# Optimization experiments

Measured on AMD Instinct MI355X. Metric: run time of the kernel, lower is better.

The kernel has to match this reference:

```python
import jax, jax.numpy as jnp
import numpy as np

N_FEATURES = 1_000_000
N_FIELDS = 50
EMB_DIM = 64
ATT_DIM = EMB_DIM // 2
BATCH = 2048


def setup_inputs() -> dict:
    key = jax.random.key(0)
    ks = jax.random.split(key, 7)
    features = jax.random.randint(ks[0], (BATCH, N_FIELDS), 0, N_FEATURES)
    emb_table = jax.random.normal(ks[1], (N_FEATURES, EMB_DIM), dtype=jnp.float32) * 0.01
    coeff_table = jax.random.normal(ks[2], (N_FEATURES, 1), dtype=jnp.float32) * 0.01
    bias = jnp.zeros((1,), dtype=jnp.float32)
    # kaiming normal for relu: std = sqrt(2/fan_in)
    att_w = jax.random.normal(ks[3], (ATT_DIM, EMB_DIM), dtype=jnp.float32) * np.sqrt(2.0 / EMB_DIM)
    att_b = jnp.zeros((ATT_DIM,), dtype=jnp.float32)
    p = jax.random.normal(ks[4], (ATT_DIM, 1), dtype=jnp.float32)
    w = jnp.ones((EMB_DIM, 1), dtype=jnp.float32)
    return {"features": features, "emb_table": emb_table, "coeff_table": coeff_table,
            "bias": bias, "att_w": att_w, "att_b": att_b, "p": p, "w": w}


def reference(features, emb_table, coeff_table, bias, att_w, att_b, p, w):
    # Dropout layers in eval mode (identity).
    emb = emb_table[features]            # [B, F, D]
    coeff = coeff_table[features]        # [B, F, 1]
    iu, ju = jnp.triu_indices(N_FIELDS, k=1)
    # pairwise hadamard products in row-major (i,j) order matching the loop
    interactions = emb[:, iu, :] * emb[:, ju, :]   # [B, P, D], P = F*(F-1)/2
    # attention MLP: relu(x @ att_w^T + att_b) @ p -> scores over interactions
    hidden = jax.nn.relu(jnp.einsum('bpd,ad->bpa', interactions, att_w) + att_b)
    scores = jnp.einsum('bpa,ao->bpo', hidden, p)  # [B, P, 1]
    att = jax.nn.softmax(scores, axis=1)           # softmax over interaction dim
    pooled = jnp.sum(interactions * att, axis=1)   # [B, D]
    interaction_part = (pooled @ w).reshape(-1)    # [B]
    linear_part = jnp.sum(coeff, axis=1).reshape(-1)
    return interaction_part + linear_part + bias
```

## Files before the change

### kernel.cpp

```cpp
#include <hip/hip_runtime.h>
#include <hip/hip_fp16.h>
#include <math.h>

#define NFIELDS 50
#define EMBD 64
#define NPAIRS 1225
#define NTILEPAD 40
#define NPAD (NTILEPAD * 32)
#define NTHREADS 256
#define NWAVES 4
#define NITER (NTILEPAD / NWAVES)
#define QPT (NPAD / NTHREADS)
#define NFPAD 51

typedef _Float16 f16x8 __attribute__((ext_vector_type(8)));
typedef _Float16 f16x2 __attribute__((ext_vector_type(2)));
typedef float f32x16 __attribute__((ext_vector_type(16)));

union F16x8U { f16x8 v; f16x2 h2[4]; unsigned int u[4]; uint4 q; };
union U32F { unsigned int u; f16x2 h; };

__device__ __forceinline__ float dot2acc(f16x2 a, f16x2 b, float c) {
#if __has_builtin(__builtin_amdgcn_fdot2)
    return __builtin_amdgcn_fdot2(a, b, c, false);
#else
    return c + (float)a[0] * (float)b[0] + (float)a[1] * (float)b[1];
#endif
}

#define MNEG (-1e30f)

__launch_bounds__(NTHREADS, 4)
__global__ void afm_kernel(const int* __restrict__ features,
                           const float* __restrict__ emb_table,
                           const float* __restrict__ coeff_table,
                           const float* __restrict__ bias,
                           const float* __restrict__ att_w,
                           const float* __restrict__ att_b,
                           const float* __restrict__ pvec,
                           const float* __restrict__ wvec,
                           float* __restrict__ out)
{
    __shared__ __align__(16) unsigned short emb3[8][NFPAD][8];
    __shared__ unsigned short pair_s[NPAD];
    __shared__ int   feat_s[NFIELDS];
    __shared__ float red_m[NWAVES], red_s[NWAVES], red_st[NWAVES];
    __shared__ float red_csum;

    const int b    = blockIdx.x;
    const int tid  = threadIdx.x;
    const int lane = tid & 63;
    const int wid  = tid >> 6;
    const int col  = lane & 31;
    const int h    = lane >> 5;
    const int h4   = h * 4;

    int myfeat = 0;
    if (tid < NFIELDS) {
        myfeat = features[b * NFIELDS + tid];
        feat_s[tid] = myfeat;
    }

    #pragma unroll
    for (int k = 0; k < QPT; ++k) {
        const int q = tid * QPT + k;
        int i = 0, j = 1;
        if (q < NPAIRS) {
            const float s = sqrtf((float)(9801 - 8 * q));
            i = (int)((99.0f - s) * 0.5f);
            const int off = i * NFIELDS - ((i * (i + 1)) >> 1);
            j = i + 1 + (q - off);
        }
        pair_s[q] = (unsigned short)((i << 8) | j);
    }

    if (wid == 0) {
        float cacc = 0.f;
        if (tid < NFIELDS)       cacc = coeff_table[myfeat];
        else if (tid == NFIELDS) cacc = bias[0];
        #pragma unroll
        for (int m = 1; m < 64; m <<= 1) cacc += __shfl_xor(cacc, m, 64);
        if (tid == 0) red_csum = cacc;
    }

    f16x8 afragW[4];
    f16x2 w2[16];
    #pragma unroll
    for (int c = 0; c < 4; ++c) {
        const int d0 = c * 16 + h * 8;
        const float4 wa0 = *reinterpret_cast<const float4*>(&att_w[col * EMBD + d0]);
        const float4 wa1 = *reinterpret_cast<const float4*>(&att_w[col * EMBD + d0 + 4]);
        F16x8U bf;
        bf.v[0] = (_Float16)wa0.x; bf.v[1] = (_Float16)wa0.y;
        bf.v[2] = (_Float16)wa0.z; bf.v[3] = (_Float16)wa0.w;
        bf.v[4] = (_Float16)wa1.x; bf.v[5] = (_Float16)wa1.y;
        bf.v[6] = (_Float16)wa1.z; bf.v[7] = (_Float16)wa1.w;
        afragW[c] = bf.v;
        const float4 wv0 = *reinterpret_cast<const float4*>(&wvec[d0]);
        const float4 wv1 = *reinterpret_cast<const float4*>(&wvec[d0 + 4]);
        f16x2 t0; t0[0] = (_Float16)wv0.x; t0[1] = (_Float16)wv0.y; w2[c * 4 + 0] = t0;
        f16x2 t1; t1[0] = (_Float16)wv0.z; t1[1] = (_Float16)wv0.w; w2[c * 4 + 1] = t1;
        f16x2 t2; t2[0] = (_Float16)wv1.x; t2[1] = (_Float16)wv1.y; w2[c * 4 + 2] = t2;
        f16x2 t3; t3[0] = (_Float16)wv1.z; t3[1] = (_Float16)wv1.w; w2[c * 4 + 3] = t3;
    }
    float attb_r[16], p_r[16];
    #pragma unroll
    for (int reg = 0; reg < 16; ++reg) {
        const int r = (reg & 3) + 8 * (reg >> 2) + 4 * h;
        attb_r[reg] = att_b[r];
        p_r[reg]    = pvec[r];
    }
    __syncthreads();

    for (int idx = tid; idx < NFIELDS * 16; idx += NTHREADS) {
        const int f  = idx >> 4;
        const int d0 = (idx & 15) * 4;
        const float4 v = *reinterpret_cast<const float4*>(
            &emb_table[(size_t)feat_s[f] * EMBD + d0]);
        const int c  = d0 >> 4;
        const int hh = (d0 >> 3) & 1;
        const int e0 = d0 & 7;
        U32F t0, t1;
        t0.h[0] = (_Float16)v.x; t0.h[1] = (_Float16)v.y;
        t1.h[0] = (_Float16)v.z; t1.h[1] = (_Float16)v.w;
        uint2 pk; pk.x = t0.u; pk.y = t1.u;
        *reinterpret_cast<uint2*>(&emb3[hh * 4 + c][f][e0]) = pk;
    }
    __syncthreads();

    float m_run = MNEG, s_run = 0.f, st_run = 0.f;

    #pragma unroll 2
    for (int tt = 0; tt < NITER; ++tt) {
        const int tile = wid + tt * NWAVES;
        const int pidx = tile * 32 + col;
        const unsigned int ij = pair_s[pidx];
        const int fi = ij >> 8;
        const int fj = ij & 255;

        f32x16 acc;
        #pragma unroll
        for (int reg = 0; reg < 16; ++reg) acc[reg] = attb_r[reg];

        float t_half = 0.f;
        #pragma unroll
        for (int c = 0; c < 4; ++c) {
            F16x8U ai, aj;
            ai.q = *reinterpret_cast<const uint4*>(&emb3[h4 + c][fi][0]);
            aj.q = *reinterpret_cast<const uint4*>(&emb3[h4 + c][fj][0]);
            const f16x2 x0 = ai.h2[0] * aj.h2[0];
            const f16x2 x1 = ai.h2[1] * aj.h2[1];
            const f16x2 x2 = ai.h2[2] * aj.h2[2];
            const f16x2 x3 = ai.h2[3] * aj.h2[3];
            t_half = dot2acc(x0, w2[c * 4 + 0], t_half);
            t_half = dot2acc(x1, w2[c * 4 + 1], t_half);
            t_half = dot2acc(x2, w2[c * 4 + 2], t_half);
            t_half = dot2acc(x3, w2[c * 4 + 3], t_half);
            F16x8U bf;
            bf.h2[0] = x0; bf.h2[1] = x1; bf.h2[2] = x2; bf.h2[3] = x3;
            acc = __builtin_amdgcn_mfma_f32_32x32x16_f16(afragW[c], bf.v, acc, 0, 0, 0);
        }

        float sp = 0.f;
        #pragma unroll
        for (int reg = 0; reg < 16; ++reg)
            sp = fmaf(fmaxf(acc[reg], 0.f), p_r[reg], sp);
        const float sc = sp + __shfl_xor(sp, 32, 64);
        const float tf = t_half + __shfl_xor(t_half, 32, 64);

        const bool valid = (pidx < NPAIRS);
        const float scm = valid ? sc : MNEG;
        const float mn  = fmaxf(m_run, scm);
        const float scale = __expf(m_run - mn);
        const float e     = valid ? __expf(sc - mn) : 0.f;
        s_run  = s_run  * scale + e;
        st_run = st_run * scale + e * tf;
        m_run  = mn;
    }

    #pragma unroll
    for (int m = 1; m < 64; m <<= 1) {
        const float m2  = __shfl_xor(m_run, m, 64);
        const float s2  = __shfl_xor(s_run, m, 64);
        const float st2 = __shfl_xor(st_run, m, 64);
        const float mn  = fmaxf(m_run, m2);
        const float ea  = __expf(m_run - mn);
        const float eb  = __expf(m2 - mn);
        s_run  = s_run * ea + s2 * eb;
        st_run = st_run * ea + st2 * eb;
        m_run  = mn;
    }
    if (lane == 0) { red_m[wid] = m_run; red_s[wid] = s_run; red_st[wid] = st_run; }
    __syncthreads();

    if (tid == 0) {
        float M = red_m[0], S = red_s[0], ST = red_st[0];
        #pragma unroll
        for (int wq = 1; wq < NWAVES; ++wq) {
            const float mn = fmaxf(M, red_m[wq]);
            const float ea = __expf(M - mn);
            const float eb = __expf(red_m[wq] - mn);
            S  = S * ea + red_s[wq] * eb;
            ST = ST * ea + red_st[wq] * eb;
            M  = mn;
        }
        out[b] = ST / S + red_csum;
    }
}

extern "C" void kernel_launch(void* const* d_in, const int* in_sizes, int n_in,
                              void* d_out, int out_size, void* d_ws, size_t ws_size,
                              hipStream_t stream) {
    const int*   features    = (const int*)d_in[0];
    const float* emb_table   = (const float*)d_in[1];
    const float* coeff_table = (const float*)d_in[2];
    const float* bias        = (const float*)d_in[3];
    const float* att_w       = (const float*)d_in[4];
    const float* att_b       = (const float*)d_in[5];
    const float* pvec        = (const float*)d_in[6];
    const float* wvec        = (const float*)d_in[7];
    float* out = (float*)d_out;

    const int batch = in_sizes[0] / NFIELDS;
    afm_kernel<<<batch, NTHREADS, 0, stream>>>(
        features, emb_table, coeff_table, bias, att_w, att_b, pvec, wvec, out);
}
```

Before: 35.94 us.

## Prefetch next tile's LDS operands and pack score epilogue into fp16 dot2

Software-pipelines the main loop: the pair index and the embedding fragments for the next tile are loaded from LDS while the current tile's MFMA runs. This hides LDS latency, at the cost of more registers and unroll 1. The epilogue is also cut down. The ReLU·p reduction now uses packed fp16 dot2 after pkrtz conversion, and the score and weighted-sum halves are packed into one 32-bit value so a single cross-half shuffle replaces two. Rounding the partial sums to fp16 lowers precision in the softmax inputs.

```diff
diff --git a/kernel.cpp b/kernel.cpp
--- a/kernel.cpp
+++ b/kernel.cpp
@@ -12,13 +12,20 @@
 #define NITER (NTILEPAD / NWAVES)
 #define QPT (NPAD / NTHREADS)
 #define NFPAD 51
+#define CHSTR (NFPAD * 8)
 
 typedef _Float16 f16x8 __attribute__((ext_vector_type(8)));
 typedef _Float16 f16x2 __attribute__((ext_vector_type(2)));
+typedef __fp16   fp16x2 __attribute__((ext_vector_type(2)));
 typedef float f32x16 __attribute__((ext_vector_type(16)));
 
 union F16x8U { f16x8 v; f16x2 h2[4]; unsigned int u[4]; uint4 q; };
-union U32F { unsigned int u; f16x2 h; };
+union U32F { unsigned int u; f16x2 h; fp16x2 g; };
+
+__device__ __forceinline__ f16x2 pkrtz(float a, float b) {
+    U32F t; t.g = __builtin_amdgcn_cvt_pkrtz(a, b);
+    return t.h;
+}
 
 __device__ __forceinline__ float dot2acc(f16x2 a, f16x2 b, float c) {
 #if __has_builtin(__builtin_amdgcn_fdot2)
@@ -103,12 +110,19 @@
         f16x2 t2; t2[0] = (_Float16)wv1.x; t2[1] = (_Float16)wv1.y; w2[c * 4 + 2] = t2;
         f16x2 t3; t3[0] = (_Float16)wv1.z; t3[1] = (_Float16)wv1.w; w2[c * 4 + 3] = t3;
     }
-    float attb_r[16], p_r[16];
+    float attb_r[16];
+    f16x2 p16[8];
     #pragma unroll
     for (int reg = 0; reg < 16; ++reg) {
         const int r = (reg & 3) + 8 * (reg >> 2) + 4 * h;
         attb_r[reg] = att_b[r];
-        p_r[reg]    = pvec[r];
+    }
+    #pragma unroll
+    for (int q = 0; q < 8; ++q) {
+        const int r0 = ((2 * q) & 3) + 8 * ((2 * q) >> 2) + 4 * h;
+        const int r1 = ((2 * q + 1) & 3) + 8 * ((2 * q + 1) >> 2) + 4 * h;
+        f16x2 pp; pp[0] = (_Float16)pvec[r0]; pp[1] = (_Float16)pvec[r1];
+        p16[q] = pp;
     }
     __syncthreads();
 
@@ -128,15 +142,38 @@
     }
     __syncthreads();
 
+    const unsigned short* const ebase = &emb3[0][0][0] + h4 * CHSTR;
+
     float m_run = MNEG, s_run = 0.f, st_run = 0.f;
 
-    #pragma unroll 2
+    uint4 ai_c[4], aj_c[4];
+    int pidx_cur = wid * 32 + col;
+    {
+        const unsigned int ij = pair_s[pidx_cur];
+        const unsigned short* pi = ebase + (ij >> 8) * 8;
+        const unsigned short* pj = ebase + (ij & 255) * 8;
+        #pragma unroll
+        for (int c = 0; c < 4; ++c) {
+            ai_c[c] = *reinterpret_cast<const uint4*>(pi + c * CHSTR);
+            aj_c[c] = *reinterpret_cast<const uint4*>(pj + c * CHSTR);
+        }
+    }
+
+    #pragma unroll 1
     for (int tt = 0; tt < NITER; ++tt) {
-        const int tile = wid + tt * NWAVES;
-        const int pidx = tile * 32 + col;
-        const unsigned int ij = pair_s[pidx];
-        const int fi = ij >> 8;
-        const int fj = ij & 255;
+        const int ttn   = (tt + 1 < NITER) ? (tt + 1) : 0;
+        const int pidx_n = (wid + ttn * NWAVES) * 32 + col;
+        uint4 ai_n[4], aj_n[4];
+        {
+            const unsigned int ijn = pair_s[pidx_n];
+            const unsigned short* pin = ebase + (ijn >> 8) * 8;
+            const unsigned short* pjn = ebase + (ijn & 255) * 8;
+            #pragma unroll
+            for (int c = 0; c < 4; ++c) {
+                ai_n[c] = *reinterpret_cast<const uint4*>(pin + c * CHSTR);
+                aj_n[c] = *reinterpret_cast<const uint4*>(pjn + c * CHSTR);
+            }
+        }
 
         f32x16 acc;
         #pragma unroll
@@ -146,8 +183,7 @@
         #pragma unroll
         for (int c = 0; c < 4; ++c) {
             F16x8U ai, aj;
-            ai.q = *reinterpret_cast<const uint4*>(&emb3[h4 + c][fi][0]);
-            aj.q = *reinterpret_cast<const uint4*>(&emb3[h4 + c][fj][0]);
+            ai.q = ai_c[c]; aj.q = aj_c[c];
             const f16x2 x0 = ai.h2[0] * aj.h2[0];
             const f16x2 x1 = ai.h2[1] * aj.h2[1];
             const f16x2 x2 = ai.h2[2] * aj.h2[2];
@@ -163,12 +199,19 @@
 
         float sp = 0.f;
         #pragma unroll
-        for (int reg = 0; reg < 16; ++reg)
-            sp = fmaf(fmaxf(acc[reg], 0.f), p_r[reg], sp);
-        const float sc = sp + __shfl_xor(sp, 32, 64);
-        const float tf = t_half + __shfl_xor(t_half, 32, 64);
-
-        const bool valid = (pidx < NPAIRS);
+        for (int q = 0; q < 8; ++q) {
+            const float r0 = fmaxf(acc[2 * q],     0.f);
+            const float r1 = fmaxf(acc[2 * q + 1], 0.f);
+            const f16x2 rr = pkrtz(r0, r1);
+            sp = dot2acc(rr, p16[q], sp);
+        }
+
+        U32F pkd; pkd.h = pkrtz(sp, t_half);
+        U32F oth; oth.u = (unsigned int)__shfl_xor((int)pkd.u, 32, 64);
+        const float sc = sp + (float)oth.h[0];
+        const float tf = t_half + (float)oth.h[1];
+
+        const bool valid = (pidx_cur < NPAIRS);
         const float scm = valid ? sc : MNEG;
         const float mn  = fmaxf(m_run, scm);
         const float scale = __expf(m_run - mn);
@@ -176,6 +219,10 @@
         s_run  = s_run  * scale + e;
         st_run = st_run * scale + e * tf;
         m_run  = mn;
+
+        #pragma unroll
+        for (int c = 0; c < 4; ++c) { ai_c[c] = ai_n[c]; aj_c[c] = aj_n[c]; }
+        pidx_cur = pidx_n;
     }
 
     #pragma unroll
```

New measurement: 39.21 us. 9.1% more time.

## Use one wave per batch row and drop block barriers and LDS reductions

Applied to the files above, without the earlier changes.

The kernel switches from four waves per batch row to a single 64-lane wave handling all 39 pair tiles. Block-level syncs become a wave barrier, and the cross-wave softmax merge through shared memory is removed. Pair indices are now computed inline instead of through an LDS table, and the feature ids are broadcast with shuffles. The two half-wave partial sums are packed into one fp16x2 shuffle, which loses precision on the exchanged halves, and each wave now does about four times the serial work.

```diff
diff --git a/kernel.cpp b/kernel.cpp
--- a/kernel.cpp
+++ b/kernel.cpp
@@ -5,20 +5,23 @@
 #define NFIELDS 50
 #define EMBD 64
 #define NPAIRS 1225
-#define NTILEPAD 40
-#define NPAD (NTILEPAD * 32)
-#define NTHREADS 256
-#define NWAVES 4
-#define NITER (NTILEPAD / NWAVES)
-#define QPT (NPAD / NTHREADS)
+#define NTILES 39
 #define NFPAD 51
+#define CHSTR (NFPAD * 8)
+#define MNEG (-1e30f)
 
 typedef _Float16 f16x8 __attribute__((ext_vector_type(8)));
 typedef _Float16 f16x2 __attribute__((ext_vector_type(2)));
+typedef __fp16   fp16x2 __attribute__((ext_vector_type(2)));
 typedef float f32x16 __attribute__((ext_vector_type(16)));
 
 union F16x8U { f16x8 v; f16x2 h2[4]; unsigned int u[4]; uint4 q; };
-union U32F { unsigned int u; f16x2 h; };
+union U32F { unsigned int u; f16x2 h; fp16x2 g; };
+
+__device__ __forceinline__ f16x2 pkrtz(float a, float b) {
+    U32F t; t.g = __builtin_amdgcn_cvt_pkrtz(a, b);
+    return t.h;
+}
 
 __device__ __forceinline__ float dot2acc(f16x2 a, f16x2 b, float c) {
 #if __has_builtin(__builtin_amdgcn_fdot2)
@@ -28,9 +31,7 @@
 #endif
 }
 
-#define MNEG (-1e30f)
-
-__launch_bounds__(NTHREADS, 4)
+__launch_bounds__(64, 2)
 __global__ void afm_kernel(const int* __restrict__ features,
                            const float* __restrict__ emb_table,
                            const float* __restrict__ coeff_table,
@@ -42,46 +43,18 @@
                            float* __restrict__ out)
 {
     __shared__ __align__(16) unsigned short emb3[8][NFPAD][8];
-    __shared__ unsigned short pair_s[NPAD];
-    __shared__ int   feat_s[NFIELDS];
-    __shared__ float red_m[NWAVES], red_s[NWAVES], red_st[NWAVES];
-    __shared__ float red_csum;
 
     const int b    = blockIdx.x;
-    const int tid  = threadIdx.x;
-    const int lane = tid & 63;
-    const int wid  = tid >> 6;
+    const int lane = threadIdx.x;
     const int col  = lane & 31;
     const int h    = lane >> 5;
     const int h4   = h * 4;
 
     int myfeat = 0;
-    if (tid < NFIELDS) {
-        myfeat = features[b * NFIELDS + tid];
-        feat_s[tid] = myfeat;
-    }
-
-    #pragma unroll
-    for (int k = 0; k < QPT; ++k) {
-        const int q = tid * QPT + k;
-        int i = 0, j = 1;
-        if (q < NPAIRS) {
-            const float s = sqrtf((float)(9801 - 8 * q));
-            i = (int)((99.0f - s) * 0.5f);
-            const int off = i * NFIELDS - ((i * (i + 1)) >> 1);
-            j = i + 1 + (q - off);
-        }
-        pair_s[q] = (unsigned short)((i << 8) | j);
-    }
-
-    if (wid == 0) {
-        float cacc = 0.f;
-        if (tid < NFIELDS)       cacc = coeff_table[myfeat];
-        else if (tid == NFIELDS) cacc = bias[0];
-        #pragma unroll
-        for (int m = 1; m < 64; m <<= 1) cacc += __shfl_xor(cacc, m, 64);
-        if (tid == 0) red_csum = cacc;
-    }
+    if (lane < NFIELDS) myfeat = features[b * NFIELDS + lane];
+    float cacc = 0.f;
+    if (lane < NFIELDS)       cacc = coeff_table[myfeat];
+    else if (lane == NFIELDS) cacc = bias[0];
 
     f16x8 afragW[4];
     f16x2 w2[16];
@@ -110,33 +83,42 @@
         attb_r[reg] = att_b[r];
         p_r[reg]    = pvec[r];
     }
-    __syncthreads();
 
-    for (int idx = tid; idx < NFIELDS * 16; idx += NTHREADS) {
-        const int f  = idx >> 4;
-        const int d0 = (idx & 15) * 4;
-        const float4 v = *reinterpret_cast<const float4*>(
-            &emb_table[(size_t)feat_s[f] * EMBD + d0]);
-        const int c  = d0 >> 4;
-        const int hh = (d0 >> 3) & 1;
-        const int e0 = d0 & 7;
-        U32F t0, t1;
-        t0.h[0] = (_Float16)v.x; t0.h[1] = (_Float16)v.y;
-        t1.h[0] = (_Float16)v.z; t1.h[1] = (_Float16)v.w;
-        uint2 pk; pk.x = t0.u; pk.y = t1.u;
-        *reinterpret_cast<uint2*>(&emb3[hh * 4 + c][f][e0]) = pk;
+    #pragma unroll
+    for (int k = 0; k < 13; ++k) {
+        const int idx = lane + k * 64;
+        if (idx < NFIELDS * 16) {
+            const int f  = idx >> 4;
+            const int d0 = (idx & 15) * 4;
+            const int ff = __shfl(myfeat, f, 64);
+            const float4 v = *reinterpret_cast<const float4*>(
+                &emb_table[(size_t)ff * EMBD + d0]);
+            const int c  = d0 >> 4;
+            const int hh = (d0 >> 3) & 1;
+            const int e0 = d0 & 7;
+            U32F t0, t1;
+            t0.h[0] = (_Float16)v.x; t0.h[1] = (_Float16)v.y;
+            t1.h[0] = (_Float16)v.z; t1.h[1] = (_Float16)v.w;
+            uint2 pk; pk.x = t0.u; pk.y = t1.u;
+            *reinterpret_cast<uint2*>(&emb3[hh * 4 + c][f][e0]) = pk;
+        }
     }
-    __syncthreads();
+    __builtin_amdgcn_wave_barrier();
 
+    const unsigned short* const ebase = &emb3[0][0][0] + h4 * CHSTR;
     float m_run = MNEG, s_run = 0.f, st_run = 0.f;
 
     #pragma unroll 2
-    for (int tt = 0; tt < NITER; ++tt) {
-        const int tile = wid + tt * NWAVES;
-        const int pidx = tile * 32 + col;
-        const unsigned int ij = pair_s[pidx];
-        const int fi = ij >> 8;
-        const int fj = ij & 255;
+    for (int tile = 0; tile < NTILES; ++tile) {
+        const int q  = tile * 32 + col;
+        const int qc = (q < NPAIRS) ? q : (NPAIRS - 1);
+        const float sq = sqrtf((float)(9801 - 8 * qc));
+        const int i   = (int)((99.0f - sq) * 0.5f);
+        const int off = i * NFIELDS - ((i * (i + 1)) >> 1);
+        const int j   = i + 1 + (qc - off);
+
+        const unsigned short* pi = ebase + i * 8;
+        const unsigned short* pj = ebase + j * 8;
 
         f32x16 acc;
         #pragma unroll
@@ -146,8 +128,8 @@
         #pragma unroll
         for (int c = 0; c < 4; ++c) {
             F16x8U ai, aj;
-            ai.q = *reinterpret_cast<const uint4*>(&emb3[h4 + c][fi][0]);
-            aj.q = *reinterpret_cast<const uint4*>(&emb3[h4 + c][fj][0]);
+            ai.q = *reinterpret_cast<const uint4*>(pi + c * CHSTR);
+            aj.q = *reinterpret_cast<const uint4*>(pj + c * CHSTR);
             const f16x2 x0 = ai.h2[0] * aj.h2[0];
             const f16x2 x1 = ai.h2[1] * aj.h2[1];
             const f16x2 x2 = ai.h2[2] * aj.h2[2];
@@ -165,10 +147,13 @@
         #pragma unroll
         for (int reg = 0; reg < 16; ++reg)
             sp = fmaf(fmaxf(acc[reg], 0.f), p_r[reg], sp);
-        const float sc = sp + __shfl_xor(sp, 32, 64);
-        const float tf = t_half + __shfl_xor(t_half, 32, 64);
 
-        const bool valid = (pidx < NPAIRS);
+        U32F pkd; pkd.h = pkrtz(sp, t_half);
+        U32F oth; oth.u = (unsigned int)__shfl_xor((int)pkd.u, 32, 64);
+        const float sc = sp + (float)oth.h[0];
+        const float tf = t_half + (float)oth.h[1];
+
+        const bool valid = (q < NPAIRS);
         const float scm = valid ? sc : MNEG;
         const float mn  = fmaxf(m_run, scm);
         const float scale = __expf(m_run - mn);
@@ -183,6 +168,7 @@
         const float m2  = __shfl_xor(m_run, m, 64);
         const float s2  = __shfl_xor(s_run, m, 64);
         const float st2 = __shfl_xor(st_run, m, 64);
+        cacc += __shfl_xor(cacc, m, 64);
         const float mn  = fmaxf(m_run, m2);
         const float ea  = __expf(m_run - mn);
         const float eb  = __expf(m2 - mn);
@@ -190,22 +176,8 @@
         st_run = st_run * ea + st2 * eb;
         m_run  = mn;
     }
-    if (lane == 0) { red_m[wid] = m_run; red_s[wid] = s_run; red_st[wid] = st_run; }
-    __syncthreads();
 
-    if (tid == 0) {
-        float M = red_m[0], S = red_s[0], ST = red_st[0];
-        #pragma unroll
-        for (int wq = 1; wq < NWAVES; ++wq) {
-            const float mn = fmaxf(M, red_m[wq]);
-            const float ea = __expf(M - mn);
-            const float eb = __expf(red_m[wq] - mn);
-            S  = S * ea + red_s[wq] * eb;
-            ST = ST * ea + red_st[wq] * eb;
-            M  = mn;
-        }
-        out[b] = ST / S + red_csum;
-    }
+    if (lane == 0) out[b] = st_run / s_run + cacc;
 }
 
 extern "C" void kernel_launch(void* const* d_in, const int* in_sizes, int n_in,
@@ -222,6 +194,6 @@
     float* out = (float*)d_out;
 
     const int batch = in_sizes[0] / NFIELDS;
-    afm_kernel<<<batch, NTHREADS, 0, stream>>>(
+    afm_kernel<<<batch, 64, 0, stream>>>(
         features, emb_table, coeff_table, bias, att_w, att_b, pvec, wvec, out);
 }
```

Result: slower. 36.92 us (+2.7%).
